# Kernel optimization log

Hardware: AMD Instinct MI355X
Metric: run time of the kernel (lower is better)

The kernel has to match this reference:

```python
import jax, jax.numpy as jnp
import numpy as np

N, E, H, ATOM, BOND, G, DEPTH = 100000, 400000, 256, 133, 14, 512, 4


def _lin(k, out_dim, in_dim):
    kw, kb = jax.random.split(k)
    s = 1.0 / np.sqrt(in_dim)
    w = jax.random.uniform(kw, (out_dim, in_dim), jnp.float32, -s, s)
    b = jax.random.uniform(kb, (out_dim,), jnp.float32, -s, s)
    return w, b


def setup_inputs() -> dict:
    key = jax.random.key(0)
    ks = jax.random.split(key, 16)
    # paired directed edges: edge 2i and 2i+1 are reverses of each other
    src_half = jax.random.randint(ks[0], (E // 2,), 0, N)
    dst_half = jax.random.randint(ks[1], (E // 2,), 0, N)
    edge_src = jnp.stack([src_half, dst_half], axis=1).reshape(-1)
    edge_dst = jnp.stack([dst_half, src_half], axis=1).reshape(-1)
    b2rev = jnp.arange(E, dtype=jnp.int64) ^ 1
    node_to_graph = jnp.sort(jax.random.randint(ks[2], (N,), 0, G))
    atom_feats = jax.random.normal(ks[3], (N, ATOM), jnp.float32)
    edge_feats = jax.random.normal(ks[4], (E, BOND), jnp.float32)
    edge_weights = jax.random.uniform(ks[5], (E,), jnp.float32)
    Wi, _ = _lin(ks[6], H, ATOM + BOND)  # W_initial, bias=False
    Wm_w, Wm_b = _lin(ks[7], H, H)
    Wn_w, Wn_b = _lin(ks[8], H, ATOM + H)
    nh0_w, nh0_b = _lin(ks[9], H, H)
    nh2_w, nh2_b = _lin(ks[10], ATOM, H)
    eh0_w, eh0_b = _lin(ks[11], H, H)
    eh2_w, eh2_b = _lin(ks[12], BOND, H)
    gh0_w, gh0_b = _lin(ks[13], H, H)
    gh2_w, gh2_b = _lin(ks[14], 1, H)
    return dict(atom_feats=atom_feats, edge_feats=edge_feats, edge_weights=edge_weights,
                Wi=Wi, Wm_w=Wm_w, Wm_b=Wm_b, Wn_w=Wn_w, Wn_b=Wn_b,
                nh0_w=nh0_w, nh0_b=nh0_b, nh2_w=nh2_w, nh2_b=nh2_b,
                eh0_w=eh0_w, eh0_b=eh0_b, eh2_w=eh2_w, eh2_b=eh2_b,
                gh0_w=gh0_w, gh0_b=gh0_b, gh2_w=gh2_w, gh2_b=gh2_b,
                edge_src=edge_src, edge_dst=edge_dst, b2rev=b2rev,
                node_to_graph=node_to_graph, depth=DEPTH, num_graphs=G)


def reference(atom_feats, edge_feats, edge_weights, Wi, Wm_w, Wm_b, Wn_w, Wn_b,
              nh0_w, nh0_b, nh2_w, nh2_b, eh0_w, eh0_b, eh2_w, eh2_b,
              gh0_w, gh0_b, gh2_w, gh2_b,
              edge_src, edge_dst, b2rev, node_to_graph, depth, num_graphs):
    Nn = atom_feats.shape[0]
    valid = b2rev >= 0
    rev_idx = jnp.where(valid, b2rev, 0)
    # initial edge hidden states: [E, H]
    h = jax.nn.relu(jnp.concatenate([atom_feats[edge_src], edge_feats], axis=1) @ Wi.T)
    for _ in range(depth):
        # weighted scatter-add of edge messages onto destination nodes: [N, H]
        M = jax.ops.segment_sum(edge_weights[:, None] * h, edge_dst, num_segments=Nn)
        rev_h = jnp.where(valid[:, None], h[rev_idx], 0.0)
        rev_w = jnp.where(valid, edge_weights[rev_idx], 0.0)
        msg = M[edge_src] - rev_w[:, None] * rev_h  # [E, H]
        h = jax.nn.relu(msg @ Wm_w.T + Wm_b)
    node_agg = jax.ops.segment_sum(edge_weights[:, None] * h, edge_dst, num_segments=Nn)
    node_repr = jax.nn.relu(jnp.concatenate([atom_feats, node_agg], axis=1) @ Wn_w.T + Wn_b)
    graph_embeds = jax.ops.segment_sum(node_repr, node_to_graph, num_segments=num_graphs)
    pred_node = jax.nn.relu(node_repr @ nh0_w.T + nh0_b) @ nh2_w.T + nh2_b
    pred_edge = jax.nn.relu(h @ eh0_w.T + eh0_b) @ eh2_w.T + eh2_b
    pred_graph = (jax.nn.relu(graph_embeds @ gh0_w.T + gh0_b) @ gh2_w.T + gh2_b).squeeze(-1)
    return (pred_node, pred_edge, pred_graph, graph_embeds, node_repr, h)
```

## Files before the change

### kernel.cpp

```cpp
#include <hip/hip_runtime.h>
#include <hip/hip_bf16.h>

#define HDIM 256
#define ATOMF 133
#define BONDF 14
#define DEPTH_HC 4
#define SCAN_CHUNK 1024
#define KWN 416

typedef short bf16x8 __attribute__((ext_vector_type(8)));
typedef float f32x4 __attribute__((ext_vector_type(4)));
typedef unsigned short u16x8 __attribute__((ext_vector_type(8)));
typedef unsigned short u16x4 __attribute__((ext_vector_type(4)));

__device__ inline float bf2f(unsigned short u) {
    unsigned int x = ((unsigned int)u) << 16;
    float f; __builtin_memcpy(&f, &x, 4); return f;
}
__device__ inline unsigned short f2bf(float f) {
    __hip_bfloat16 h = __float2bfloat16(f);
    unsigned short u; __builtin_memcpy(&u, &h, 2); return u;
}

__device__ inline void gload_lds16(const unsigned short* g, unsigned short* lds) {
    __builtin_amdgcn_global_load_lds(
        (const __attribute__((address_space(1))) unsigned int*)g,
        (__attribute__((address_space(3))) unsigned int*)lds, 16, 0, 0);
}

#define MFMA_STEP(ASB, BSB)                                                        \
    {                                                                              \
        const int kq = (l >> 4) * 8;                                               \
        const int rbase = (wr << 6) + (l & 15);                                    \
        const int cbase = (wc << 6) + (l & 15);                                    \
        bf16x8 af[4], bfr[4];                                                      \
        _Pragma("unroll")                                                          \
        for (int i = 0; i < 4; ++i) {                                              \
            af[i]  = *(const bf16x8*)&(ASB)[(rbase + i * 16) * 32 + kq];           \
            bfr[i] = *(const bf16x8*)&(BSB)[(cbase + i * 16) * 32 + kq];           \
        }                                                                          \
        _Pragma("unroll")                                                          \
        for (int mi = 0; mi < 4; ++mi)                                             \
            _Pragma("unroll")                                                      \
            for (int ni = 0; ni < 4; ++ni)                                         \
                acc[mi][ni] = __builtin_amdgcn_mfma_f32_16x16x32_bf16(             \
                    af[mi], bfr[ni], acc[mi][ni], 0, 0, 0);                        \
    }

__global__ __launch_bounds__(512) void mfma_gemm_cat(
    const unsigned short* __restrict__ atomb,
    const float* __restrict__ bond,
    const int* __restrict__ src, int E,
    const unsigned short* __restrict__ W,
    unsigned short* __restrict__ Cb)
{
    __shared__ unsigned short As[2][128 * 32];
    __shared__ unsigned short Bs[2][256 * 32];
    const int t = threadIdx.x;
    const int w = t >> 6, l = t & 63;
    const int m0 = blockIdx.x * 128;
    const int wr = w >> 2, wc = w & 3;

    f32x4 acc[4][4] = {};

    const int ar = t >> 2;
    const int ac0 = (t & 3) * 8;
    long long e_row = m0 + ar; if (e_row > E - 1) e_row = E - 1;
    const int sn = src[e_row];
    const unsigned short* arow = atomb + (size_t)sn * 160;
    const float* brow = bond + (size_t)e_row * BONDF;

    u16x8 tail = *(const u16x8*)&arow[128 + ac0];
    #pragma unroll
    for (int i = 0; i < 8; ++i) {
        int k = 128 + ac0 + i;
        if (k >= ATOMF && k < ATOMF + BONDF) tail[i] = f2bf(brow[k - ATOMF]);
    }

    const int kcol = (l & 3) * 8;
    const int rowL = (w << 4) + (l >> 2);

    {
        u16x8 o = *(const u16x8*)&arow[ac0];
        *(u16x8*)&As[0][ar * 32 + ac0] = o;
        gload_lds16(W + (size_t)rowL * 160 + kcol, Bs[0] + (size_t)w * 512);
        gload_lds16(W + (size_t)(128 + rowL) * 160 + kcol, Bs[0] + 4096 + (size_t)w * 512);
    }
    u16x8 regs = *(const u16x8*)&arow[32 + ac0];
    __syncthreads();

    #pragma unroll
    for (int c = 0; c < 5; ++c) {
        const int cb = c & 1, nb = cb ^ 1;
        if (c + 1 < 5) {
            u16x8 o = (c + 1 == 4) ? tail : regs;
            *(u16x8*)&As[nb][ar * 32 + ac0] = o;
            gload_lds16(W + (size_t)rowL * 160 + (c + 1) * 32 + kcol, Bs[nb] + (size_t)w * 512);
            gload_lds16(W + (size_t)(128 + rowL) * 160 + (c + 1) * 32 + kcol,
                        Bs[nb] + 4096 + (size_t)w * 512);
            if (c + 2 < 4) regs = *(const u16x8*)&arow[(c + 2) * 32 + ac0];
        }
        MFMA_STEP(As[cb], Bs[cb]);
        __syncthreads();
    }

    const int ccol = l & 15, crow = (l >> 4) * 4;
    #pragma unroll
    for (int ni = 0; ni < 4; ++ni) {
        int gn = (wc << 6) + ni * 16 + ccol;
        #pragma unroll
        for (int mi = 0; mi < 4; ++mi) {
            #pragma unroll
            for (int j = 0; j < 4; ++j) {
                long long gm = m0 + (wr << 6) + mi * 16 + crow + j;
                if (gm >= E) continue;
                float v = fmaxf(acc[mi][ni][j], 0.0f);
                Cb[(size_t)gm * HDIM + gn] = f2bf(v);
            }
        }
    }
}

__global__ __launch_bounds__(512) void mfma_gemm_msg(
    const unsigned short* __restrict__ Mb,
    unsigned short* h,
    const float* __restrict__ w,
    const int* __restrict__ src, int E,
    const unsigned short* __restrict__ W,
    const float* __restrict__ bias,
    float* __restrict__ Cf)
{
    __shared__ unsigned short As[2][128 * 32];
    __shared__ unsigned short Bs[2][256 * 32];
    const int t = threadIdx.x;
    const int wv = t >> 6, l = t & 63;
    const int m0 = blockIdx.x * 128;
    const int wr = wv >> 2, wc = wv & 3;

    f32x4 acc[4][4] = {};

    const int ar = t >> 2;
    const int ac0 = (t & 3) * 8;
    long long e_row = m0 + ar; if (e_row > E - 1) e_row = E - 1;
    const long long er1 = e_row ^ 1;
    const int sn = src[e_row];
    const float we1 = w[er1];
    const unsigned short* mrow = Mb + (size_t)sn * HDIM;
    const unsigned short* hrow = h + (size_t)er1 * HDIM;

    const int kcol = (l & 3) * 8;
    const int rowL = (wv << 4) + (l >> 2);

    {
        u16x8 Mv = *(const u16x8*)&mrow[ac0];
        u16x8 hv = *(const u16x8*)&hrow[ac0];
        u16x8 o;
        #pragma unroll
        for (int i = 0; i < 8; ++i) o[i] = f2bf(bf2f(Mv[i]) - we1 * bf2f(hv[i]));
        *(u16x8*)&As[0][ar * 32 + ac0] = o;
        gload_lds16(W + (size_t)rowL * 256 + kcol, Bs[0] + (size_t)wv * 512);
        gload_lds16(W + (size_t)(128 + rowL) * 256 + kcol, Bs[0] + 4096 + (size_t)wv * 512);
    }
    u16x8 Mr = *(const u16x8*)&mrow[32 + ac0];
    u16x8 hr = *(const u16x8*)&hrow[32 + ac0];
    __syncthreads();

    #pragma unroll
    for (int c = 0; c < 8; ++c) {
        const int cb = c & 1, nb = cb ^ 1;
        if (c + 1 < 8) {
            u16x8 o;
            #pragma unroll
            for (int i = 0; i < 8; ++i) o[i] = f2bf(bf2f(Mr[i]) - we1 * bf2f(hr[i]));
            *(u16x8*)&As[nb][ar * 32 + ac0] = o;
            gload_lds16(W + (size_t)rowL * 256 + (c + 1) * 32 + kcol, Bs[nb] + (size_t)wv * 512);
            gload_lds16(W + (size_t)(128 + rowL) * 256 + (c + 1) * 32 + kcol,
                        Bs[nb] + 4096 + (size_t)wv * 512);
            if (c + 2 < 8) {
                Mr = *(const u16x8*)&mrow[(c + 2) * 32 + ac0];
                hr = *(const u16x8*)&hrow[(c + 2) * 32 + ac0];
            }
        }
        MFMA_STEP(As[cb], Bs[cb]);
        __syncthreads();
    }

    const int ccol = l & 15, crow = (l >> 4) * 4;
    #pragma unroll
    for (int ni = 0; ni < 4; ++ni) {
        int gn = (wc << 6) + ni * 16 + ccol;
        float bv = bias[gn];
        #pragma unroll
        for (int mi = 0; mi < 4; ++mi) {
            #pragma unroll
            for (int j = 0; j < 4; ++j) {
                long long gm = m0 + (wr << 6) + mi * 16 + crow + j;
                if (gm >= E) continue;
                float v = fmaxf(acc[mi][ni][j] + bv, 0.0f);
                if (Cf) Cf[(size_t)gm * HDIM + gn] = v;
                h[(size_t)gm * HDIM + gn] = f2bf(v);
            }
        }
    }
}

__global__ __launch_bounds__(512) void mfma_gemm_catwn(
    const unsigned short* __restrict__ atomb,
    const unsigned short* __restrict__ Mb,
    int N,
    const unsigned short* __restrict__ W,
    const float* __restrict__ bias,
    float* __restrict__ Cf,
    unsigned short* __restrict__ Cb)
{
    __shared__ unsigned short As[2][128 * 32];
    __shared__ unsigned short Bs[2][256 * 32];
    const int t = threadIdx.x;
    const int wv = t >> 6, l = t & 63;
    const int m0 = blockIdx.x * 128;
    const int wr = wv >> 2, wc = wv & 3;

    f32x4 acc[4][4] = {};

    const int ar = t >> 2;
    const int ac0 = (t & 3) * 8;
    long long nrow = m0 + ar; if (nrow > N - 1) nrow = N - 1;
    const unsigned short* arow = atomb + (size_t)nrow * 160;
    const unsigned short* mrow = Mb + (size_t)nrow * HDIM;

    const int kcol = (l & 3) * 8;
    const int rowL = (wv << 4) + (l >> 2);

    #define LOADA_WN(c) ((c) < 5 ? *(const u16x8*)&arow[(c) * 32 + ac0] \
                                 : *(const u16x8*)&mrow[(c) * 32 - 160 + ac0])

    {
        u16x8 o = LOADA_WN(0);
        *(u16x8*)&As[0][ar * 32 + ac0] = o;
        gload_lds16(W + (size_t)rowL * KWN + kcol, Bs[0] + (size_t)wv * 512);
        gload_lds16(W + (size_t)(128 + rowL) * KWN + kcol, Bs[0] + 4096 + (size_t)wv * 512);
    }
    u16x8 regs = LOADA_WN(1);
    __syncthreads();

    #pragma unroll
    for (int c = 0; c < 13; ++c) {
        const int cb = c & 1, nb = cb ^ 1;
        if (c + 1 < 13) {
            *(u16x8*)&As[nb][ar * 32 + ac0] = regs;
            gload_lds16(W + (size_t)rowL * KWN + (c + 1) * 32 + kcol, Bs[nb] + (size_t)wv * 512);
            gload_lds16(W + (size_t)(128 + rowL) * KWN + (c + 1) * 32 + kcol,
                        Bs[nb] + 4096 + (size_t)wv * 512);
            if (c + 2 < 13) regs = LOADA_WN(c + 2);
        }
        MFMA_STEP(As[cb], Bs[cb]);
        __syncthreads();
    }
    #undef LOADA_WN

    const int ccol = l & 15, crow = (l >> 4) * 4;
    #pragma unroll
    for (int ni = 0; ni < 4; ++ni) {
        int gn = (wc << 6) + ni * 16 + ccol;
        float bv = bias[gn];
        #pragma unroll
        for (int mi = 0; mi < 4; ++mi) {
            #pragma unroll
            for (int j = 0; j < 4; ++j) {
                long long gm = m0 + (wr << 6) + mi * 16 + crow + j;
                if (gm >= N) continue;
                float v = fmaxf(acc[mi][ni][j] + bv, 0.0f);
                Cf[(size_t)gm * HDIM + gn] = v;
                Cb[(size_t)gm * HDIM + gn] = f2bf(v);
            }
        }
    }
}

__global__ __launch_bounds__(512) void head_fused(
    const unsigned short* __restrict__ A, int Mrows,
    const unsigned short* __restrict__ W,
    const float* __restrict__ b0,
    const unsigned short* __restrict__ W2b,
    const float* __restrict__ b2,
    float* __restrict__ pred, int NOUT2)
{
    __shared__ unsigned short R[128 * 256];
    unsigned short* As0 = R;
    unsigned short* As1 = R + 4096;
    unsigned short* Bs0 = R + 8192;
    unsigned short* Bs1 = R + 16384;
    unsigned short* AsB[2] = {As0, As1};
    unsigned short* BsB[2] = {Bs0, Bs1};
    const int t = threadIdx.x;
    const int w = t >> 6, l = t & 63;
    const int m0 = blockIdx.x * 128;
    const int wr = w >> 2, wc = w & 3;
    const int kq = (l >> 4) * 8;

    f32x4 acc[4][4] = {};
    const int kcol = (l & 3) * 8;
    const int rowL = (w << 4) + (l >> 2);
    long long r0 = m0 + rowL; if (r0 > Mrows - 1) r0 = Mrows - 1;

    {
        gload_lds16(A + (size_t)r0 * 256 + kcol, As0 + (size_t)w * 512);
        gload_lds16(W + (size_t)rowL * 256 + kcol, Bs0 + (size_t)w * 512);
        gload_lds16(W + (size_t)(128 + rowL) * 256 + kcol, Bs0 + 4096 + (size_t)w * 512);
    }
    __syncthreads();

    #pragma unroll
    for (int c = 0; c < 8; ++c) {
        const int cb = c & 1, nb = cb ^ 1;
        if (c + 1 < 8) {
            gload_lds16(A + (size_t)r0 * 256 + (c + 1) * 32 + kcol, AsB[nb] + (size_t)w * 512);
            gload_lds16(W + (size_t)rowL * 256 + (c + 1) * 32 + kcol, BsB[nb] + (size_t)w * 512);
            gload_lds16(W + (size_t)(128 + rowL) * 256 + (c + 1) * 32 + kcol,
                        BsB[nb] + 4096 + (size_t)w * 512);
        }
        MFMA_STEP(AsB[cb], BsB[cb]);
        __syncthreads();
    }

    const int ccol = l & 15, crow = (l >> 4) * 4;
    #pragma unroll
    for (int ni = 0; ni < 4; ++ni) {
        const int col = (wc << 6) + ni * 16 + ccol;
        const float bv = b0[col];
        #pragma unroll
        for (int mi = 0; mi < 4; ++mi) {
            #pragma unroll
            for (int j = 0; j < 4; ++j) {
                const int rr = (wr << 6) + mi * 16 + crow + j;
                float v = fmaxf(acc[mi][ni][j] + bv, 0.0f);
                size_t byteoff = ((size_t)rr * 512 + (size_t)col * 2) ^ (size_t)((rr & 7) << 4);
                *(unsigned short*)((char*)R + byteoff) = f2bf(v);
            }
        }
    }
    __syncthreads();

    const int erow = (w << 4) + (l & 15);
    const int jrow = l & 15;
    for (int cc = 0; cc * 16 < NOUT2; ++cc) {
        bf16x8 w2b[8];
        #pragma unroll
        for (int ks = 0; ks < 8; ++ks)
            w2b[ks] = *(const bf16x8*)&W2b[(size_t)(cc * 16 + jrow) * 256 + ks * 32 + kq];
        f32x4 acc2 = {};
        #pragma unroll
        for (int ks = 0; ks < 8; ++ks) {
            size_t byteoff = ((size_t)erow * 512 + (size_t)(ks * 64 + kq * 2))
                             ^ (size_t)((erow & 7) << 4);
            bf16x8 af;
            __builtin_memcpy(&af, (char*)R + byteoff, 16);
            acc2 = __builtin_amdgcn_mfma_f32_16x16x32_bf16(af, w2b[ks], acc2, 0, 0, 0);
        }
        const int col = cc * 16 + jrow;
        if (col < NOUT2) {
            #pragma unroll
            for (int j = 0; j < 4; ++j) {
                long long gm = m0 + (w << 4) + (l >> 4) * 4 + j;
                if (gm < Mrows) pred[gm * NOUT2 + col] = acc2[j] + b2[col];
            }
        }
    }
}

__global__ __launch_bounds__(640) void atom_conv(const float* __restrict__ a,
                                                 unsigned short* __restrict__ ab, int N) {
    int n = blockIdx.x * 4 + threadIdx.x / 160;
    int c = threadIdx.x % 160;
    if (n >= N) return;
    ab[(size_t)n * 160 + c] = (c < ATOMF) ? f2bf(a[(size_t)n * ATOMF + c]) : (unsigned short)0;
}

__global__ void pad_all(const float* Wi, const float* Wm, const float* Wn,
                        const float* n0, const float* n2, const float* e0, const float* e2,
                        unsigned short* Wib, unsigned short* Wmb, unsigned short* Wnb,
                        unsigned short* n0b, unsigned short* n2b, unsigned short* e0b,
                        unsigned short* e2b) {
    int wid = blockIdx.x >> 8;
    int r = blockIdx.x & 255;
    if (wid == 2) {
        for (int c = threadIdx.x; c < KWN; c += blockDim.x) {
            float v = 0.0f;
            if (c < ATOMF)      v = Wn[(size_t)r * 389 + c];
            else if (c >= 160)  v = Wn[(size_t)r * 389 + (c - 27)];
            Wnb[(size_t)r * KWN + c] = f2bf(v);
        }
        return;
    }
    const float* S; unsigned short* D; int R, C, Cp;
    switch (wid) {
        case 0: S = Wi; D = Wib; R = 256; C = 147; Cp = 160; break;
        case 1: S = Wm; D = Wmb; R = 256; C = 256; Cp = 256; break;
        case 3: S = n0; D = n0b; R = 256; C = 256; Cp = 256; break;
        case 4: S = n2; D = n2b; R = 133; C = 256; Cp = 256; break;
        case 5: S = e0; D = e0b; R = 256; C = 256; Cp = 256; break;
        default: S = e2; D = e2b; R = 14;  C = 256; Cp = 256; break;
    }
    for (int c = threadIdx.x; c < Cp; c += blockDim.x) {
        float v = (r < R && c < C) ? S[(size_t)r * C + c] : 0.0f;
        D[(size_t)r * Cp + c] = f2bf(v);
    }
}

__global__ void count_dst(const int* __restrict__ dst, int* __restrict__ cnt, int E) {
    int e = blockIdx.x * 256 + threadIdx.x;
    if (e < E) atomicAdd(&cnt[dst[e]], 1);
}

__global__ void scan_reduce(const int* __restrict__ cnt, int* __restrict__ csum, int n) {
    __shared__ int s[256];
    int base = blockIdx.x * SCAN_CHUNK;
    int v = 0;
    for (int i = threadIdx.x; i < SCAN_CHUNK; i += 256) {
        int idx = base + i;
        v += (idx < n) ? cnt[idx] : 0;
    }
    s[threadIdx.x] = v; __syncthreads();
    for (int o = 128; o > 0; o >>= 1) {
        if (threadIdx.x < o) s[threadIdx.x] += s[threadIdx.x + o];
        __syncthreads();
    }
    if (threadIdx.x == 0) csum[blockIdx.x] = s[0];
}

__global__ void scan_sums(const int* __restrict__ csum, int* __restrict__ coff, int nchunks) {
    __shared__ int s[1024];
    int t = threadIdx.x;
    s[t] = (t < nchunks) ? csum[t] : 0;
    __syncthreads();
    for (int o = 1; o < 1024; o <<= 1) {
        int v = (t >= o) ? s[t - o] : 0;
        __syncthreads();
        s[t] += v;
        __syncthreads();
    }
    if (t < nchunks) coff[t] = (t == 0) ? 0 : s[t - 1];
}

__global__ void scan_apply(const int* __restrict__ cnt, const int* __restrict__ coff,
                           int* __restrict__ off, int* __restrict__ cursor, int n) {
    __shared__ int s[256];
    int b = blockIdx.x, t = threadIdx.x;
    if (b == 0 && t == 0) off[0] = 0;
    int base = b * SCAN_CHUNK + t * 4;
    int v[4];
    #pragma unroll
    for (int i = 0; i < 4; ++i) v[i] = (base + i < n) ? cnt[base + i] : 0;
    s[t] = v[0] + v[1] + v[2] + v[3];
    __syncthreads();
    for (int o = 1; o < 256; o <<= 1) {
        int x = (t >= o) ? s[t - o] : 0;
        __syncthreads();
        s[t] += x;
        __syncthreads();
    }
    int run = coff[b] + ((t > 0) ? s[t - 1] : 0);
    #pragma unroll
    for (int i = 0; i < 4; ++i) {
        if (base + i < n) cursor[base + i] = run;
        run += v[i];
        if (base + i < n) off[base + i + 1] = run;
    }
}

__global__ void fill_elist(const int* __restrict__ dst, int* __restrict__ cursor,
                           int* __restrict__ elist, int E) {
    int e = blockIdx.x * 256 + threadIdx.x;
    if (e < E) {
        int p = atomicAdd(&cursor[dst[e]], 1);
        elist[p] = e;
    }
}

__global__ void sort_buckets(const int* __restrict__ off, int* __restrict__ elist, int N) {
    int n = blockIdx.x * 256 + threadIdx.x;
    if (n >= N) return;
    int s = off[n], t = off[n + 1];
    for (int i = s; i < t - 1; ++i) {
        int mn = elist[i], mi = i;
        for (int j = i + 1; j < t; ++j) {
            int v = elist[j];
            if (v < mn) { mn = v; mi = j; }
        }
        if (mi != i) { elist[mi] = elist[i]; elist[i] = mn; }
    }
}

__global__ void gather_M(const unsigned short* __restrict__ h, const float* __restrict__ w,
                         const int* __restrict__ off, const int* __restrict__ elist,
                         unsigned short* __restrict__ Mb, int N) {
    int n = blockIdx.x * 4 + (threadIdx.x >> 6);
    if (n >= N) return;
    int c = (threadIdx.x & 63) * 4;
    int s = off[n], e_ = off[n + 1];
    float4 acc = {0.f, 0.f, 0.f, 0.f};
    for (int i = s; i < e_; i += 4) {
        int m = e_ - i;
        int f[4]; float wf[4]; u16x4 hv[4];
        #pragma unroll
        for (int j = 0; j < 4; ++j) if (j < m) f[j] = elist[i + j];
        #pragma unroll
        for (int j = 0; j < 4; ++j) if (j < m) {
            wf[j] = w[f[j]];
            hv[j] = *(const u16x4*)&h[(size_t)f[j] * HDIM + c];
        }
        #pragma unroll
        for (int j = 0; j < 4; ++j) if (j < m) {
            acc.x += wf[j] * bf2f(hv[j][0]);
            acc.y += wf[j] * bf2f(hv[j][1]);
            acc.z += wf[j] * bf2f(hv[j][2]);
            acc.w += wf[j] * bf2f(hv[j][3]);
        }
    }
    u16x4 o;
    o[0] = f2bf(acc.x); o[1] = f2bf(acc.y); o[2] = f2bf(acc.z); o[3] = f2bf(acc.w);
    *(u16x4*)&Mb[(size_t)n * HDIM + c] = o;
}

__global__ void graph_sum(const float* __restrict__ nr, const int* __restrict__ n2g,
                          float* __restrict__ ge, int N) {
    int g = blockIdx.x, t = threadIdx.x;
    int lo = 0, hi = N;
    while (lo < hi) { int mid = (lo + hi) >> 1; if (n2g[mid] < g) lo = mid + 1; else hi = mid; }
    int start = lo;
    hi = N;
    while (lo < hi) { int mid = (lo + hi) >> 1; if (n2g[mid] < g + 1) lo = mid + 1; else hi = mid; }
    int end = lo;
    float acc = 0.0f;
    for (int n = start; n < end; ++n) acc += nr[(size_t)n * HDIM + t];
    ge[(size_t)g * HDIM + t] = acc;
}

__global__ __launch_bounds__(256) void graph_head(
    const float* __restrict__ ge,
    const float* __restrict__ w0, const float* __restrict__ b0,
    const float* __restrict__ w2, const float* __restrict__ b2,
    float* __restrict__ pred, int G)
{
    int g = blockIdx.x;
    if (g >= G) return;
    __shared__ float xs[256];
    __shared__ float ys[256];
    int t = threadIdx.x;
    xs[t] = ge[(size_t)g * 256 + t];
    __syncthreads();
    float acc = b0[t];
    const float* wr = w0 + (size_t)t * 256;
    #pragma unroll 8
    for (int k = 0; k < 256; ++k) acc = fmaf(wr[k], xs[k], acc);
    ys[t] = fmaxf(acc, 0.0f) * w2[t];
    __syncthreads();
    for (int o = 128; o > 0; o >>= 1) {
        if (t < o) ys[t] += ys[t + o];
        __syncthreads();
    }
    if (t == 0) pred[g] = ys[0] + b2[0];
}

extern "C" void kernel_launch(void* const* d_in, const int* in_sizes, int n_in,
                              void* d_out, int out_size, void* d_ws, size_t ws_size,
                              hipStream_t stream) {
    const float* atom_feats   = (const float*)d_in[0];
    const float* edge_feats   = (const float*)d_in[1];
    const float* edge_weights = (const float*)d_in[2];
    const float* Wi    = (const float*)d_in[3];
    const float* Wm_w  = (const float*)d_in[4];
    const float* Wm_b  = (const float*)d_in[5];
    const float* Wn_w  = (const float*)d_in[6];
    const float* Wn_b  = (const float*)d_in[7];
    const float* nh0_w = (const float*)d_in[8];
    const float* nh0_b = (const float*)d_in[9];
    const float* nh2_w = (const float*)d_in[10];
    const float* nh2_b = (const float*)d_in[11];
    const float* eh0_w = (const float*)d_in[12];
    const float* eh0_b = (const float*)d_in[13];
    const float* eh2_w = (const float*)d_in[14];
    const float* eh2_b = (const float*)d_in[15];
    const float* gh0_w = (const float*)d_in[16];
    const float* gh0_b = (const float*)d_in[17];
    const float* gh2_w = (const float*)d_in[18];
    const float* gh2_b = (const float*)d_in[19];
    const int* edge_src      = (const int*)d_in[20];
    const int* edge_dst      = (const int*)d_in[21];
    const int* node_to_graph = (const int*)d_in[23];

    int N = in_sizes[0] / ATOMF;
    int E = in_sizes[1] / BONDF;
    long long G = ((long long)out_size - (long long)N * (ATOMF + HDIM)
                   - (long long)E * (BONDF + HDIM)) / (1 + HDIM);

    float* out = (float*)d_out;
    float* pred_node = out;
    float* pred_edge = pred_node + (size_t)N * ATOMF;
    float* pred_grph = pred_edge + (size_t)E * BONDF;
    float* gemb      = pred_grph + (size_t)G;
    float* node_repr = gemb + (size_t)G * HDIM;
    float* h_f32     = node_repr + (size_t)N * HDIM;

    unsigned short* hA    = (unsigned short*)d_ws;
    unsigned short* nrb   = hA + (size_t)E * HDIM;
    unsigned short* Mb    = nrb + (size_t)N * HDIM;
    unsigned short* atomb = Mb + (size_t)N * HDIM;
    unsigned short* Wib   = atomb + (size_t)N * 160;
    unsigned short* Wmb   = Wib + 256 * 160;
    unsigned short* Wnb   = Wmb + 256 * 256;
    unsigned short* nh0b  = Wnb + 256 * KWN;
    unsigned short* nh2b  = nh0b + 256 * 256;
    unsigned short* eh0b  = nh2b + 256 * 256;
    unsigned short* eh2b  = eh0b + 256 * 256;
    int* csr = (int*)(eh2b + 256 * 256);
    int* cnt    = csr;
    int* off    = cnt + N;
    int* cursor = off + N + 1;
    int* elist  = cursor + N;
    int* csum   = elist + E;
    int* coff   = csum + 1024;

    int nchunks = (N + SCAN_CHUNK - 1) / SCAN_CHUNK;

    hipMemsetAsync(cnt, 0, (size_t)N * sizeof(int), stream);
    count_dst<<<(E + 255) / 256, 256, 0, stream>>>(edge_dst, cnt, E);
    scan_reduce<<<nchunks, 256, 0, stream>>>(cnt, csum, N);
    scan_sums<<<1, 1024, 0, stream>>>(csum, coff, nchunks);
    scan_apply<<<nchunks, 256, 0, stream>>>(cnt, coff, off, cursor, N);
    fill_elist<<<(E + 255) / 256, 256, 0, stream>>>(edge_dst, cursor, elist, E);
    sort_buckets<<<(N + 255) / 256, 256, 0, stream>>>(off, elist, N);

    pad_all<<<7 * 256, 256, 0, stream>>>(Wi, Wm_w, Wn_w, nh0_w, nh2_w, eh0_w, eh2_w,
                                         Wib, Wmb, Wnb, nh0b, nh2b, eh0b, eh2b);
    atom_conv<<<(N + 3) / 4, 640, 0, stream>>>(atom_feats, atomb, N);

    mfma_gemm_cat<<<(E + 127) / 128, 512, 0, stream>>>(atomb, edge_feats, edge_src,
                                                       E, Wib, hA);

    int ngrid = (N + 3) / 4;
    for (int d = 0; d < DEPTH_HC; ++d) {
        gather_M<<<ngrid, 256, 0, stream>>>(hA, edge_weights, off, elist, Mb, N);
        float* cf = (d == DEPTH_HC - 1) ? h_f32 : nullptr;
        mfma_gemm_msg<<<(E + 127) / 128, 512, 0, stream>>>(
            Mb, hA, edge_weights, edge_src, E, Wmb, Wm_b, cf);
    }

    head_fused<<<(E + 127) / 128, 512, 0, stream>>>(hA, E, eh0b, eh0_b, eh2b, eh2_b,
                                                    pred_edge, BONDF);

    gather_M<<<ngrid, 256, 0, stream>>>(hA, edge_weights, off, elist, Mb, N);
    mfma_gemm_catwn<<<(N + 127) / 128, 512, 0, stream>>>(atomb, Mb, N, Wnb, Wn_b,
                                                         node_repr, nrb);

    graph_sum<<<(int)G, HDIM, 0, stream>>>(node_repr, node_to_graph, gemb, N);

    head_fused<<<(N + 127) / 128, 512, 0, stream>>>(nrb, N, nh0b, nh0_b, nh2b, nh2_b,
                                                    pred_node, ATOMF);

    graph_head<<<(int)G, 256, 0, stream>>>(gemb, gh0_w, gh0_b, gh2_w, gh2_b,
                                           pred_grph, (int)G);
}
```

Baseline: 1.789 ms.

## Deepen message GEMM pipeline with register-staged fragments and single barrier per step

```diff
diff --git a/kernel.cpp b/kernel.cpp
--- a/kernel.cpp
+++ b/kernel.cpp
@@ -152,37 +152,82 @@
     const int rowL = (wv << 4) + (l >> 2);
 
     {
-        u16x8 Mv = *(const u16x8*)&mrow[ac0];
-        u16x8 hv = *(const u16x8*)&hrow[ac0];
-        u16x8 o;
-        #pragma unroll
-        for (int i = 0; i < 8; ++i) o[i] = f2bf(bf2f(Mv[i]) - we1 * bf2f(hv[i]));
-        *(u16x8*)&As[0][ar * 32 + ac0] = o;
+        u16x8 M0 = *(const u16x8*)&mrow[ac0];
+        u16x8 h0 = *(const u16x8*)&hrow[ac0];
+        u16x8 M1 = *(const u16x8*)&mrow[32 + ac0];
+        u16x8 h1 = *(const u16x8*)&hrow[32 + ac0];
+        u16x8 o0, o1;
+        #pragma unroll
+        for (int i = 0; i < 8; ++i) {
+            o0[i] = f2bf(bf2f(M0[i]) - we1 * bf2f(h0[i]));
+            o1[i] = f2bf(bf2f(M1[i]) - we1 * bf2f(h1[i]));
+        }
+        *(u16x8*)&As[0][ar * 32 + ac0] = o0;
+        *(u16x8*)&As[1][ar * 32 + ac0] = o1;
         gload_lds16(W + (size_t)rowL * 256 + kcol, Bs[0] + (size_t)wv * 512);
         gload_lds16(W + (size_t)(128 + rowL) * 256 + kcol, Bs[0] + 4096 + (size_t)wv * 512);
-    }
-    u16x8 Mr = *(const u16x8*)&mrow[32 + ac0];
-    u16x8 hr = *(const u16x8*)&hrow[32 + ac0];
-    __syncthreads();
+        gload_lds16(W + (size_t)rowL * 256 + 32 + kcol, Bs[1] + (size_t)wv * 512);
+        gload_lds16(W + (size_t)(128 + rowL) * 256 + 32 + kcol, Bs[1] + 4096 + (size_t)wv * 512);
+    }
+    u16x8 Mra = *(const u16x8*)&mrow[64 + ac0];
+    u16x8 hra = *(const u16x8*)&hrow[64 + ac0];
+    u16x8 Mrb = *(const u16x8*)&mrow[96 + ac0];
+    u16x8 hrb = *(const u16x8*)&hrow[96 + ac0];
+    asm volatile("s_waitcnt lgkmcnt(0)" ::: "memory");
+    asm volatile("s_waitcnt vmcnt(4)" ::: "memory");
+    __builtin_amdgcn_sched_barrier(0);
+    __builtin_amdgcn_s_barrier();
+    asm volatile("" ::: "memory");
+    __builtin_amdgcn_sched_barrier(0);
+
+    const int kq = (l >> 4) * 8;
+    const int rbase = (wr << 6) + (l & 15);
+    const int cbase = (wc << 6) + (l & 15);
 
     #pragma unroll
     for (int c = 0; c < 8; ++c) {
-        const int cb = c & 1, nb = cb ^ 1;
-        if (c + 1 < 8) {
+        const int cb = c & 1;
+        bf16x8 af[4], bfr[4];
+        #pragma unroll
+        for (int i = 0; i < 4; ++i) {
+            af[i]  = *(const bf16x8*)&As[cb][(rbase + i * 16) * 32 + kq];
+            bfr[i] = *(const bf16x8*)&Bs[cb][(cbase + i * 16) * 32 + kq];
+        }
+        asm volatile("s_waitcnt lgkmcnt(0)" ::: "memory");
+        __builtin_amdgcn_sched_barrier(0);
+        if (c <= 4) { asm volatile("s_waitcnt vmcnt(2)" ::: "memory"); }
+        else        { asm volatile("s_waitcnt vmcnt(0)" ::: "memory"); }
+        __builtin_amdgcn_sched_barrier(0);
+        __builtin_amdgcn_s_barrier();
+        asm volatile("" ::: "memory");
+        __builtin_amdgcn_sched_barrier(0);
+        if (c + 2 < 8) {
+            u16x8 Mu = (c & 1) ? Mrb : Mra;
+            u16x8 hu = (c & 1) ? hrb : hra;
             u16x8 o;
             #pragma unroll
-            for (int i = 0; i < 8; ++i) o[i] = f2bf(bf2f(Mr[i]) - we1 * bf2f(hr[i]));
-            *(u16x8*)&As[nb][ar * 32 + ac0] = o;
-            gload_lds16(W + (size_t)rowL * 256 + (c + 1) * 32 + kcol, Bs[nb] + (size_t)wv * 512);
-            gload_lds16(W + (size_t)(128 + rowL) * 256 + (c + 1) * 32 + kcol,
-                        Bs[nb] + 4096 + (size_t)wv * 512);
-            if (c + 2 < 8) {
-                Mr = *(const u16x8*)&mrow[(c + 2) * 32 + ac0];
-                hr = *(const u16x8*)&hrow[(c + 2) * 32 + ac0];
+            for (int i = 0; i < 8; ++i) o[i] = f2bf(bf2f(Mu[i]) - we1 * bf2f(hu[i]));
+            *(u16x8*)&As[cb][ar * 32 + ac0] = o;
+            gload_lds16(W + (size_t)rowL * 256 + (c + 2) * 32 + kcol,
+                        Bs[cb] + (size_t)wv * 512);
+            gload_lds16(W + (size_t)(128 + rowL) * 256 + (c + 2) * 32 + kcol,
+                        Bs[cb] + 4096 + (size_t)wv * 512);
+            if (c + 4 < 8) {
+                if (c & 1) {
+                    Mrb = *(const u16x8*)&mrow[(c + 4) * 32 + ac0];
+                    hrb = *(const u16x8*)&hrow[(c + 4) * 32 + ac0];
+                } else {
+                    Mra = *(const u16x8*)&mrow[(c + 4) * 32 + ac0];
+                    hra = *(const u16x8*)&hrow[(c + 4) * 32 + ac0];
+                }
             }
         }
-        MFMA_STEP(As[cb], Bs[cb]);
-        __syncthreads();
+        #pragma unroll
+        for (int mi = 0; mi < 4; ++mi)
+            #pragma unroll
+            for (int ni = 0; ni < 4; ++ni)
+                acc[mi][ni] = __builtin_amdgcn_mfma_f32_16x16x32_bf16(
+                    af[mi], bfr[ni], acc[mi][ni], 0, 0, 0);
     }
 
     const int ccol = l & 15, crow = (l >> 4) * 4;
```

After: 1.912 ms. 6.9% more time.
